# Optimization experiments

Measured on AMD Instinct MI355X. Metric: run time of the kernel, lower is better.

Reference implementation:

```python
import jax, jax.numpy as jnp
import numpy as np

NUM_EMBEDDINGS = 1024
EMBEDDING_DIM = 64


def setup_inputs() -> dict:
    key = jax.random.key(0)
    kx, kw = jax.random.split(key)
    x = jax.random.normal(kx, (16, 4096, EMBEDDING_DIM), dtype=jnp.float32)
    # torch init: uniform(-1/K, 1/K)
    bound = 1.0 / NUM_EMBEDDINGS
    weight = jax.random.uniform(kw, (NUM_EMBEDDINGS, EMBEDDING_DIM),
                                dtype=jnp.float32, minval=-bound, maxval=bound)
    return {"x": x, "weight": weight}


def reference(x, weight):
    flat_x = x.reshape(-1, EMBEDDING_DIM)                      # [N, D]
    x_sq = jnp.sum(flat_x ** 2, axis=1, keepdims=True)
    w_sq = jnp.sum(weight ** 2, axis=1)[None, :]
    distances = x_sq - 2.0 * (flat_x @ weight.T) + w_sq
    encoding_indices = jnp.argmin(distances, axis=1)           # [N]
    quantized = weight[encoding_indices]                       # [N, D]
    e_latent_loss = jnp.mean((jax.lax.stop_gradient(quantized) - flat_x) ** 2)
    q_latent_loss = jnp.mean((quantized - jax.lax.stop_gradient(flat_x)) ** 2)
    loss = q_latent_loss + 0.25 * e_latent_loss
    # straight-through estimator
    quantized = flat_x + jax.lax.stop_gradient(quantized - flat_x)
    return quantized.reshape(x.shape), encoding_indices, loss
```

## Files before the change

kernel.cpp:

```cpp
#include <hip/hip_runtime.h>
#include <math.h>

#define EMB_D 64
#define MARGIN 6.0e-5f
#define SBIAS 0.5f

typedef float  f32x4  __attribute__((ext_vector_type(4)));
typedef short  bf16x8 __attribute__((ext_vector_type(8)));

__device__ __forceinline__ unsigned short f2bf(float f) {
    unsigned int u = __float_as_uint(f);
    return (unsigned short)((u + 0x7FFFu + ((u >> 16) & 1u)) >> 16);
}
__device__ __forceinline__ float bf2f(unsigned short h) {
    return __uint_as_float(((unsigned int)h) << 16);
}

union Pack8 { ushort u[8]; bf16x8 v; uint4 q; };

__device__ __forceinline__ bf16x8 ldbf8(const unsigned short* p) {
    union { uint4 u; bf16x8 v; } c;
    c.u = *(const uint4*)p;
    return c.v;
}

__global__ __launch_bounds__(256)
void vq_prepw_kernel(const float* __restrict__ w,
                     unsigned short* __restrict__ wt_hi,
                     unsigned short* __restrict__ wt_lo,
                     float* __restrict__ wsq, float* __restrict__ loss_out,
                     int K) {
    const int i = blockIdx.x * 256 + threadIdx.x;
    if (i == 0) loss_out[0] = 0.f;
    if (i >= K * 8) return;
    const int krow = i >> 3, q = i & 7;
    const int dest = ((krow >> 6) << 9) + (((krow >> 4) & 3) << 7) + (q << 4)
                   + (krow & 15);
    const float* src = w + (size_t)krow * EMB_D + q * 8;
    Pack8 h, l;
#pragma unroll
    for (int j = 0; j < 8; ++j) {
        const float f = src[j];
        h.u[j] = f2bf(f);
        l.u[j] = f2bf(f - bf2f(h.u[j]));
    }
    ((uint4*)wt_hi)[dest] = h.q;
    ((uint4*)wt_lo)[dest] = l.q;

    if (i < K) {
        const float* wr = w + (size_t)i * EMB_D;
        float r[8];
#pragma unroll
        for (int j = 0; j < 8; ++j) r[j] = __fmul_rn(wr[j], wr[j]);
#pragma unroll
        for (int t = 1; t < 8; ++t)
#pragma unroll
            for (int j = 0; j < 8; ++j)
                r[j] = __fadd_rn(r[j], __fmul_rn(wr[t * 8 + j], wr[t * 8 + j]));
        float a = __fadd_rn(__fadd_rn(r[0], r[1]), __fadd_rn(r[2], r[3]));
        float b = __fadd_rn(__fadd_rn(r[4], r[5]), __fadd_rn(r[6], r[7]));
        wsq[i] = __fadd_rn(a, b);
    }
}

__global__ __launch_bounds__(256, 2)
void vq_fused_kernel(const float* __restrict__ x,
                     const unsigned short* __restrict__ wt_hi,
                     const unsigned short* __restrict__ wt_lo,
                     const float* __restrict__ wsq,
                     const float* __restrict__ w,
                     float* __restrict__ out, float* __restrict__ loss_out,
                     int K, int N, float scale) {
    const int tid  = threadIdx.x;
    const int lane = tid & 63;
    const int wave = tid >> 6;
    const int quad = lane >> 4;
    const int c16  = lane & 15;
    const int rowbase = blockIdx.x * 64 + wave * 16;

    __shared__ uint4 sh4[512];
    __shared__ uint4 sl4[512];
    __shared__ float wsq_lds[1024];
    __shared__ unsigned Mp1[4][16][17];
    __shared__ unsigned Mp2[4][16][17];
    __shared__ int kf[64], strow[64], k2row[64];

    const float* xrow = x + (size_t)(rowbase + c16) * EMB_D + quad * 8;
    Pack8 ah0, al0, ah1, al1;
#pragma unroll
    for (int j = 0; j < 8; ++j) {
        const float f0 = xrow[j];
        ah0.u[j] = f2bf(f0); al0.u[j] = f2bf(f0 - bf2f(ah0.u[j]));
        const float f1 = xrow[32 + j];
        ah1.u[j] = f2bf(f1); al1.u[j] = f2bf(f1 - bf2f(ah1.u[j]));
    }
    const bf16x8 AH0 = ah0.v, AL0 = al0.v, AH1 = ah1.v, AL1 = al1.v;

    {
        float4 a = ((const float4*)wsq)[tid];
        a.x += SBIAS; a.y += SBIAS; a.z += SBIAS; a.w += SBIAS;
        ((float4*)wsq_lds)[tid] = a;
    }

    unsigned s1v[4], s2v[4];
#pragma unroll
    for (int i = 0; i < 4; ++i) { s1v[i] = 0xFFFFFFFFu; s2v[i] = 0xFFFFFFFFu; }

    const uint4* gh = (const uint4*)wt_hi;
    const uint4* gl = (const uint4*)wt_lo;
    uint4 ph0 = gh[tid], ph1 = gh[256 + tid];
    uint4 pl0 = gl[tid], pl1 = gl[256 + tid];

    const int nseg = K >> 6;
    for (int seg = 0; seg < nseg; ++seg) {
        sh4[tid] = ph0; sh4[256 + tid] = ph1;
        sl4[tid] = pl0; sl4[256 + tid] = pl1;
        __syncthreads();
        if (seg + 1 < nseg) {
            const int b = (seg + 1) * 512;
            ph0 = gh[b + tid]; ph1 = gh[b + 256 + tid];
            pl0 = gl[b + tid]; pl1 = gl[b + 256 + tid];
        }

#pragma unroll
        for (int s = 0; s < 4; ++s) {
            const unsigned short* shp = (const unsigned short*)sh4;
            const unsigned short* slp = (const unsigned short*)sl4;
            const bf16x8 bhi0 = ldbf8(shp + (s * 128 + lane) * 8);
            const bf16x8 bhi1 = ldbf8(shp + (s * 128 + 64 + lane) * 8);
            const bf16x8 blo0 = ldbf8(slp + (s * 128 + lane) * 8);
            const bf16x8 blo1 = ldbf8(slp + (s * 128 + 64 + lane) * 8);
            const float wqb = wsq_lds[seg * 64 + s * 16 + c16];
            const unsigned idx6 = (unsigned)(seg * 4 + s);

            f32x4 a0 = {0.f, 0.f, 0.f, 0.f};
            f32x4 a1 = {0.f, 0.f, 0.f, 0.f};
            a0 = __builtin_amdgcn_mfma_f32_16x16x32_bf16(AL0, bhi0, a0, 0, 0, 0);
            a1 = __builtin_amdgcn_mfma_f32_16x16x32_bf16(AL1, bhi1, a1, 0, 0, 0);
            a0 = __builtin_amdgcn_mfma_f32_16x16x32_bf16(AH0, blo0, a0, 0, 0, 0);
            a1 = __builtin_amdgcn_mfma_f32_16x16x32_bf16(AH1, blo1, a1, 0, 0, 0);
            a0 = __builtin_amdgcn_mfma_f32_16x16x32_bf16(AH0, bhi0, a0, 0, 0, 0);
            a1 = __builtin_amdgcn_mfma_f32_16x16x32_bf16(AH1, bhi1, a1, 0, 0, 0);
#pragma unroll
            for (int i = 0; i < 4; ++i) {
                const float sc = fmaf(-2.0f, a0[i] + a1[i], wqb);
                const unsigned p = (__float_as_uint(sc) & 0xFFFFFFC0u) | idx6;
                const unsigned mx = p > s1v[i] ? p : s1v[i];
                s2v[i] = s2v[i] < mx ? s2v[i] : mx;
                s1v[i] = s1v[i] < p  ? s1v[i] : p;
            }
        }
        __syncthreads();
    }

#pragma unroll
    for (int i = 0; i < 4; ++i) {
        Mp1[wave][quad * 4 + i][c16] = s1v[i];
        Mp2[wave][quad * 4 + i][c16] = s2v[i];
    }
    __syncthreads();
    if (tid < 64) {
        const int wv = tid >> 4, r = tid & 15;
        unsigned g1 = 0xFFFFFFFFu, g2 = 0xFFFFFFFFu, g3 = 0xFFFFFFFFu;
        int gk1 = 0, gk2 = 0;
#pragma unroll
        for (int c = 0; c < 16; ++c) {
            {
                const unsigned p = Mp1[wv][r][c];
                if (p < g1)      { g3 = g2; g2 = g1; gk2 = gk1; g1 = p;
                                   gk1 = (int)(((p & 63u) << 4) | (unsigned)c); }
                else if (p < g2) { g3 = g2; g2 = p;
                                   gk2 = (int)(((p & 63u) << 4) | (unsigned)c); }
                else if (p < g3) { g3 = p; }
            }
            {
                const unsigned p = Mp2[wv][r][c];
                if (p < g1)      { g3 = g2; g2 = g1; gk2 = gk1; g1 = p;
                                   gk1 = (int)(((p & 63u) << 4) | (unsigned)c); }
                else if (p < g2) { g3 = g2; g2 = p;
                                   gk2 = (int)(((p & 63u) << 4) | (unsigned)c); }
                else if (p < g3) { g3 = p; }
            }
        }
        kf[tid] = gk1;
        const float f1 = __uint_as_float(g1 & 0xFFFFFFC0u);
        const float f2 = __uint_as_float(g2 & 0xFFFFFFC0u);
        const float f3 = __uint_as_float(g3 & 0xFFFFFFC0u);
        int st = 0;
        if (f2 - f1 <= MARGIN) st = (f3 - f1 > MARGIN) ? 1 : 2;
        strow[tid] = st;
        k2row[tid] = gk2;
    }
    __syncthreads();

    if (tid < 64 && strow[tid] == 1) {
        const int row = blockIdx.x * 64 + tid;
        const int ka = kf[tid], kb = k2row[tid];
        const float4* xp = (const float4*)(x + (size_t)row * EMB_D);
        const float4* wa = (const float4*)(w + (size_t)ka * EMB_D);
        const float4* wb = (const float4*)(w + (size_t)kb * EMB_D);
        float r[8];
        double aa0 = 0, aa1 = 0, aa2 = 0, aa3 = 0;
        double ab0 = 0, ab1 = 0, ab2 = 0, ab3 = 0;
#pragma unroll
        for (int q = 0; q < 16; ++q) {
            const float4 xv = xp[q], va = wa[q], vb = wb[q];
            const int j = (q & 1) * 4;
            if (q < 2) {
                r[j + 0] = __fmul_rn(xv.x, xv.x);
                r[j + 1] = __fmul_rn(xv.y, xv.y);
                r[j + 2] = __fmul_rn(xv.z, xv.z);
                r[j + 3] = __fmul_rn(xv.w, xv.w);
            } else {
                r[j + 0] = __fadd_rn(r[j + 0], __fmul_rn(xv.x, xv.x));
                r[j + 1] = __fadd_rn(r[j + 1], __fmul_rn(xv.y, xv.y));
                r[j + 2] = __fadd_rn(r[j + 2], __fmul_rn(xv.z, xv.z));
                r[j + 3] = __fadd_rn(r[j + 3], __fmul_rn(xv.w, xv.w));
            }
            aa0 = fma((double)xv.x, (double)va.x, aa0);
            aa1 = fma((double)xv.y, (double)va.y, aa1);
            aa2 = fma((double)xv.z, (double)va.z, aa2);
            aa3 = fma((double)xv.w, (double)va.w, aa3);
            ab0 = fma((double)xv.x, (double)vb.x, ab0);
            ab1 = fma((double)xv.y, (double)vb.y, ab1);
            ab2 = fma((double)xv.z, (double)vb.z, ab2);
            ab3 = fma((double)xv.w, (double)vb.w, ab3);
        }
        const float xsq = __fadd_rn(
            __fadd_rn(__fadd_rn(r[0], r[1]), __fadd_rn(r[2], r[3])),
            __fadd_rn(__fadd_rn(r[4], r[5]), __fadd_rn(r[6], r[7])));
        const float mfa = (float)((aa0 + aa1) + (aa2 + aa3));
        const float mfb = (float)((ab0 + ab1) + (ab2 + ab3));
        const float sa = __fadd_rn(__fsub_rn(xsq, __fmul_rn(2.0f, mfa)), wsq[ka]);
        const float sb = __fadd_rn(__fsub_rn(xsq, __fmul_rn(2.0f, mfb)), wsq[kb]);
        int win = ka;
        if (sb < sa || (sb == sa && kb < ka)) win = kb;
        kf[tid] = win;
    }
    __syncthreads();

    __shared__ float4 xs4[16];
    __shared__ float  xsqs;
    __shared__ float  ls[256];
    __shared__ int    lk[256];
    for (int i = 0; i < 64; ++i) {
        if (strow[i] != 2) continue;
        const int row = blockIdx.x * 64 + i;
        if (tid < 16) xs4[tid] = ((const float4*)(x + (size_t)row * EMB_D))[tid];
        __syncthreads();
        if (tid == 0) {
            const float* xf = (const float*)xs4;
            float r[8];
#pragma unroll
            for (int j = 0; j < 8; ++j) r[j] = __fmul_rn(xf[j], xf[j]);
#pragma unroll
            for (int t = 1; t < 8; ++t)
#pragma unroll
                for (int j = 0; j < 8; ++j)
                    r[j] = __fadd_rn(r[j], __fmul_rn(xf[t * 8 + j], xf[t * 8 + j]));
            xsqs = __fadd_rn(
                __fadd_rn(__fadd_rn(r[0], r[1]), __fadd_rn(r[2], r[3])),
                __fadd_rn(__fadd_rn(r[4], r[5]), __fadd_rn(r[6], r[7])));
        }
        __syncthreads();
        const float xsq = xsqs;

        float bs = INFINITY;
        int   bk = K;
        for (int t = 0; t < 4; ++t) {
            const int k = wave * (K >> 2) + t * 64 + lane;
            const float4* wr4 = (const float4*)(w + (size_t)k * EMB_D);
            double a0 = 0.0, a1 = 0.0, a2 = 0.0, a3 = 0.0;
#pragma unroll
            for (int q = 0; q < EMB_D / 4; ++q) {
                const float4 xv = xs4[q];
                const float4 wv = wr4[q];
                a0 = fma((double)xv.x, (double)wv.x, a0);
                a1 = fma((double)xv.y, (double)wv.y, a1);
                a2 = fma((double)xv.z, (double)wv.z, a2);
                a3 = fma((double)xv.w, (double)wv.w, a3);
            }
            const float mf = (float)((a0 + a1) + (a2 + a3));
            const float t2 = __fsub_rn(xsq, __fmul_rn(2.0f, mf));
            const float sc = __fadd_rn(t2, wsq[k]);
            if (sc < bs || (sc == bs && k < bk)) { bs = sc; bk = k; }
        }
        ls[tid] = bs; lk[tid] = bk;
        __syncthreads();
        if (wave == 0) {
            float gs = ls[lane];
            int   gk = lk[lane];
#pragma unroll
            for (int c = 1; c < 4; ++c) {
                const float os = ls[c * 64 + lane];
                const int   ok = lk[c * 64 + lane];
                if (os < gs || (os == gs && ok < gk)) { gs = os; gk = ok; }
            }
#pragma unroll
            for (int off = 32; off > 0; off >>= 1) {
                const float os = __shfl_down(gs, off);
                const int   ok = __shfl_down(gk, off);
                if (os < gs || (os == gs && ok < gk)) { gs = os; gk = ok; }
            }
            if (lane == 0) kf[i] = gk;
        }
        __syncthreads();
    }

    if (tid < 64) {
        const int row = blockIdx.x * 64 + tid;
        out[(size_t)N * EMB_D + row] = (float)kf[tid];
    }
    float lpart = 0.f;
#pragma unroll
    for (int rep = 0; rep < 4; ++rep) {
        int f4   = rep * 256 + tid;
        int rr   = f4 >> 4;
        int c    = f4 & 15;
        int k    = kf[rr];
        int grow = blockIdx.x * 64 + rr;
        float4 wv = ((const float4*)(w + (size_t)k * EMB_D))[c];
        float4 xq = ((const float4*)(x + (size_t)grow * EMB_D))[c];
        ((float4*)out)[(size_t)grow * (EMB_D / 4) + c] = wv;
        float dx = wv.x - xq.x, dy = wv.y - xq.y;
        float dz = wv.z - xq.z, dw = wv.w - xq.w;
        lpart += dx * dx + dy * dy + dz * dz + dw * dw;
    }
#pragma unroll
    for (int off = 32; off > 0; off >>= 1) lpart += __shfl_down(lpart, off);
    __shared__ float lred[4];
    if (lane == 0) lred[wave] = lpart;
    __syncthreads();
    if (tid == 0)
        atomicAdd(loss_out, ((lred[0] + lred[1]) + (lred[2] + lred[3])) * scale);
}

extern "C" void kernel_launch(void* const* d_in, const int* in_sizes, int n_in,
                              void* d_out, int out_size, void* d_ws, size_t ws_size,
                              hipStream_t stream) {
    const float* x = (const float*)d_in[0];
    const float* w = (const float*)d_in[1];
    float* out = (float*)d_out;
    const int xsz = in_sizes[0];
    const int wsz = in_sizes[1];
    const int N   = xsz / EMB_D;
    const int K   = wsz / EMB_D;
    const int NB  = N / 64;
    float* loss_out = out + (size_t)N * EMB_D + N;

    float* wsq = (float*)d_ws;
    unsigned short* wt_hi = (unsigned short*)(wsq + K);
    unsigned short* wt_lo = wt_hi + (size_t)K * EMB_D;

    vq_prepw_kernel<<<(K * 8 + 255) / 256, 256, 0, stream>>>(w, wt_hi, wt_lo,
                                                             wsq, loss_out, K);
    vq_fused_kernel<<<NB, 256, 0, stream>>>(x, wt_hi, wt_lo, wsq, w, out,
                                            loss_out, K, N,
                                            1.25f / (float)xsz);
}
```

Measured before the change: 134.4 us.

## Double-buffer codebook tiles in LDS via direct global-to-LDS loads

Replaces register-staged prefetch of the bf16 hi/lo codebook tiles with `global_load_lds` 16-byte direct transfers into a two-slot LDS arena. The next segment is fetched into the alternate buffer while the current one is consumed. This aims to remove the register round-trip and the per-segment LDS store instructions, and to cut VGPR pressure. The Mp1/Mp2 scratch arrays now alias the arena to limit LDS growth. The cost is more LDS per block and a correctness dependence on waitcnt and barrier placement for the asynchronous LDS writes.

```diff
diff --git a/kernel.cpp b/kernel.cpp
--- a/kernel.cpp
+++ b/kernel.cpp
@@ -22,6 +22,12 @@
     union { uint4 u; bf16x8 v; } c;
     c.u = *(const uint4*)p;
     return c.v;
+}
+
+__device__ __forceinline__ void stage16(const void* g, void* l) {
+    __builtin_amdgcn_global_load_lds(
+        (const __attribute__((address_space(1))) unsigned int*)g,
+        (__attribute__((address_space(3))) unsigned int*)l, 16, 0, 0);
 }
 
 __global__ __launch_bounds__(256)
@@ -78,12 +84,24 @@
     const int c16  = lane & 15;
     const int rowbase = blockIdx.x * 64 + wave * 16;
 
-    __shared__ uint4 sh4[512];
-    __shared__ uint4 sl4[512];
+    __shared__ __align__(16) char arena[32768];
     __shared__ float wsq_lds[1024];
-    __shared__ unsigned Mp1[4][16][17];
-    __shared__ unsigned Mp2[4][16][17];
+    typedef unsigned MpArr[16][17];
+    MpArr* Mp1 = (MpArr*)arena;
+    MpArr* Mp2 = (MpArr*)(arena + 4352);
     __shared__ int kf[64], strow[64], k2row[64];
+
+    const uint4* gh4 = (const uint4*)wt_hi;
+    const uint4* gl4 = (const uint4*)wt_lo;
+
+    {
+        uint4* bh = (uint4*)arena;
+        uint4* bl = (uint4*)(arena + 8192);
+        stage16(gh4 + tid,       bh + tid);
+        stage16(gh4 + 256 + tid, bh + 256 + tid);
+        stage16(gl4 + tid,       bl + tid);
+        stage16(gl4 + 256 + tid, bl + 256 + tid);
+    }
 
     const float* xrow = x + (size_t)(rowbase + c16) * EMB_D + quad * 8;
     Pack8 ah0, al0, ah1, al1;
@@ -106,26 +124,27 @@
 #pragma unroll
     for (int i = 0; i < 4; ++i) { s1v[i] = 0xFFFFFFFFu; s2v[i] = 0xFFFFFFFFu; }
 
-    const uint4* gh = (const uint4*)wt_hi;
-    const uint4* gl = (const uint4*)wt_lo;
-    uint4 ph0 = gh[tid], ph1 = gh[256 + tid];
-    uint4 pl0 = gl[tid], pl1 = gl[256 + tid];
+    __syncthreads();
 
     const int nseg = K >> 6;
     for (int seg = 0; seg < nseg; ++seg) {
-        sh4[tid] = ph0; sh4[256 + tid] = ph1;
-        sl4[tid] = pl0; sl4[256 + tid] = pl1;
-        __syncthreads();
+        const int cur = seg & 1;
         if (seg + 1 < nseg) {
             const int b = (seg + 1) * 512;
-            ph0 = gh[b + tid]; ph1 = gh[b + 256 + tid];
-            pl0 = gl[b + tid]; pl1 = gl[b + 256 + tid];
-        }
+            uint4* bh = (uint4*)(arena + (cur ^ 1) * 16384);
+            uint4* bl = (uint4*)(arena + (cur ^ 1) * 16384 + 8192);
+            stage16(gh4 + b + tid,       bh + tid);
+            stage16(gh4 + b + 256 + tid, bh + 256 + tid);
+            stage16(gl4 + b + tid,       bl + tid);
+            stage16(gl4 + b + 256 + tid, bl + 256 + tid);
+        }
+
+        const unsigned short* shp =
+            (const unsigned short*)(arena + cur * 16384);
+        const unsigned short* slp = shp + 4096;
 
 #pragma unroll
         for (int s = 0; s < 4; ++s) {
-            const unsigned short* shp = (const unsigned short*)sh4;
-            const unsigned short* slp = (const unsigned short*)sl4;
             const bf16x8 bhi0 = ldbf8(shp + (s * 128 + lane) * 8);
             const bf16x8 bhi1 = ldbf8(shp + (s * 128 + 64 + lane) * 8);
             const bf16x8 blo0 = ldbf8(slp + (s * 128 + lane) * 8);
```

Measured after the change: 139.3 us. 1.04x slower.

## Split codebook across wave pairs and give each wave two row tiles

Applied to the files above, without the earlier changes.

Each wave now handles 32 rows (two 16-row tiles) against half of the codebook, instead of 16 rows against the whole codebook. Every B fragment read from LDS feeds two sets of MFMAs, which halves LDS reads per MFMA. The staging loop drops from 16 segments of 64 codes to 16 steps of 32 codes per half, and the final merge combines the two halves. Register pressure roughly doubles for the A fragments and the top-2 state, which may hurt occupancy. Code and step counts are hardcoded to K=1024.

```diff
diff --git a/kernel.cpp b/kernel.cpp
--- a/kernel.cpp
+++ b/kernel.cpp
@@ -76,25 +76,32 @@
     const int wave = tid >> 6;
     const int quad = lane >> 4;
     const int c16  = lane & 15;
-    const int rowbase = blockIdx.x * 64 + wave * 16;
-
-    __shared__ uint4 sh4[512];
-    __shared__ uint4 sl4[512];
+    const int h    = wave >> 1;
+    const int rg   = wave & 1;
+    const int rowbase = blockIdx.x * 64 + rg * 32;
+
+    __shared__ __align__(16) char arena[17408];
     __shared__ float wsq_lds[1024];
-    __shared__ unsigned Mp1[4][16][17];
-    __shared__ unsigned Mp2[4][16][17];
+    typedef unsigned MpArr[32][17];
+    MpArr* Mp1 = (MpArr*)arena;
+    MpArr* Mp2 = (MpArr*)(arena + 8704);
     __shared__ int kf[64], strow[64], k2row[64];
 
-    const float* xrow = x + (size_t)(rowbase + c16) * EMB_D + quad * 8;
-    Pack8 ah0, al0, ah1, al1;
-#pragma unroll
-    for (int j = 0; j < 8; ++j) {
-        const float f0 = xrow[j];
-        ah0.u[j] = f2bf(f0); al0.u[j] = f2bf(f0 - bf2f(ah0.u[j]));
-        const float f1 = xrow[32 + j];
-        ah1.u[j] = f2bf(f1); al1.u[j] = f2bf(f1 - bf2f(ah1.u[j]));
-    }
-    const bf16x8 AH0 = ah0.v, AL0 = al0.v, AH1 = ah1.v, AL1 = al1.v;
+    Pack8 AH0[2], AL0[2], AH1[2], AL1[2];
+#pragma unroll
+    for (int tt = 0; tt < 2; ++tt) {
+        const float* xrow =
+            x + (size_t)(rowbase + tt * 16 + c16) * EMB_D + quad * 8;
+#pragma unroll
+        for (int j = 0; j < 8; ++j) {
+            const float f0 = xrow[j];
+            AH0[tt].u[j] = f2bf(f0);
+            AL0[tt].u[j] = f2bf(f0 - bf2f(AH0[tt].u[j]));
+            const float f1 = xrow[32 + j];
+            AH1[tt].u[j] = f2bf(f1);
+            AL1[tt].u[j] = f2bf(f1 - bf2f(AH1[tt].u[j]));
+        }
+    }
 
     {
         float4 a = ((const float4*)wsq)[tid];
@@ -102,84 +109,100 @@
         ((float4*)wsq_lds)[tid] = a;
     }
 
-    unsigned s1v[4], s2v[4];
-#pragma unroll
-    for (int i = 0; i < 4; ++i) { s1v[i] = 0xFFFFFFFFu; s2v[i] = 0xFFFFFFFFu; }
-
-    const uint4* gh = (const uint4*)wt_hi;
-    const uint4* gl = (const uint4*)wt_lo;
-    uint4 ph0 = gh[tid], ph1 = gh[256 + tid];
-    uint4 pl0 = gl[tid], pl1 = gl[256 + tid];
-
-    const int nseg = K >> 6;
-    for (int seg = 0; seg < nseg; ++seg) {
-        sh4[tid] = ph0; sh4[256 + tid] = ph1;
-        sl4[tid] = pl0; sl4[256 + tid] = pl1;
-        __syncthreads();
-        if (seg + 1 < nseg) {
-            const int b = (seg + 1) * 512;
-            ph0 = gh[b + tid]; ph1 = gh[b + 256 + tid];
-            pl0 = gl[b + tid]; pl1 = gl[b + 256 + tid];
-        }
-
-#pragma unroll
-        for (int s = 0; s < 4; ++s) {
-            const unsigned short* shp = (const unsigned short*)sh4;
-            const unsigned short* slp = (const unsigned short*)sl4;
+    unsigned s1v[2][4], s2v[2][4];
+#pragma unroll
+    for (int tt = 0; tt < 2; ++tt)
+#pragma unroll
+        for (int i = 0; i < 4; ++i) { s1v[tt][i] = 0xFFFFFFFFu; s2v[tt][i] = 0xFFFFFFFFu; }
+
+    const uint4* gh4 = (const uint4*)wt_hi;
+    const uint4* gl4 = (const uint4*)wt_lo;
+    uint4 ph0 = gh4[tid], pl0 = gl4[tid];
+    uint4 ph1 = gh4[4096 + tid], pl1 = gl4[4096 + tid];
+
+    for (int t = 0; t < 16; ++t) {
+        ((uint4*)arena)[tid]           = ph0;
+        ((uint4*)(arena + 4096))[tid]  = pl0;
+        ((uint4*)(arena + 8192))[tid]  = ph1;
+        ((uint4*)(arena + 12288))[tid] = pl1;
+        __syncthreads();
+        if (t + 1 < 16) {
+            ph0 = gh4[(t + 1) * 256 + tid];
+            pl0 = gl4[(t + 1) * 256 + tid];
+            ph1 = gh4[(17 + t) * 256 + tid];
+            pl1 = gl4[(17 + t) * 256 + tid];
+        }
+
+        const unsigned short* shp =
+            (const unsigned short*)(arena + h * 8192);
+        const unsigned short* slp = shp + 2048;
+
+#pragma unroll
+        for (int s = 0; s < 2; ++s) {
             const bf16x8 bhi0 = ldbf8(shp + (s * 128 + lane) * 8);
             const bf16x8 bhi1 = ldbf8(shp + (s * 128 + 64 + lane) * 8);
             const bf16x8 blo0 = ldbf8(slp + (s * 128 + lane) * 8);
             const bf16x8 blo1 = ldbf8(slp + (s * 128 + 64 + lane) * 8);
-            const float wqb = wsq_lds[seg * 64 + s * 16 + c16];
-            const unsigned idx6 = (unsigned)(seg * 4 + s);
-
-            f32x4 a0 = {0.f, 0.f, 0.f, 0.f};
-            f32x4 a1 = {0.f, 0.f, 0.f, 0.f};
-            a0 = __builtin_amdgcn_mfma_f32_16x16x32_bf16(AL0, bhi0, a0, 0, 0, 0);
-            a1 = __builtin_amdgcn_mfma_f32_16x16x32_bf16(AL1, bhi1, a1, 0, 0, 0);
-            a0 = __builtin_amdgcn_mfma_f32_16x16x32_bf16(AH0, blo0, a0, 0, 0, 0);
-            a1 = __builtin_amdgcn_mfma_f32_16x16x32_bf16(AH1, blo1, a1, 0, 0, 0);
-            a0 = __builtin_amdgcn_mfma_f32_16x16x32_bf16(AH0, bhi0, a0, 0, 0, 0);
-            a1 = __builtin_amdgcn_mfma_f32_16x16x32_bf16(AH1, bhi1, a1, 0, 0, 0);
-#pragma unroll
-            for (int i = 0; i < 4; ++i) {
-                const float sc = fmaf(-2.0f, a0[i] + a1[i], wqb);
-                const unsigned p = (__float_as_uint(sc) & 0xFFFFFFC0u) | idx6;
-                const unsigned mx = p > s1v[i] ? p : s1v[i];
-                s2v[i] = s2v[i] < mx ? s2v[i] : mx;
-                s1v[i] = s1v[i] < p  ? s1v[i] : p;
-            }
-        }
-        __syncthreads();
-    }
-
-#pragma unroll
-    for (int i = 0; i < 4; ++i) {
-        Mp1[wave][quad * 4 + i][c16] = s1v[i];
-        Mp2[wave][quad * 4 + i][c16] = s2v[i];
-    }
+            const unsigned u = (unsigned)(h * 32 + t * 2 + s);
+            const float wqb = wsq_lds[u * 16 + c16];
+
+#pragma unroll
+            for (int tt = 0; tt < 2; ++tt) {
+                f32x4 a0 = {0.f, 0.f, 0.f, 0.f};
+                f32x4 a1 = {0.f, 0.f, 0.f, 0.f};
+                a0 = __builtin_amdgcn_mfma_f32_16x16x32_bf16(AL0[tt].v, bhi0, a0, 0, 0, 0);
+                a1 = __builtin_amdgcn_mfma_f32_16x16x32_bf16(AL1[tt].v, bhi1, a1, 0, 0, 0);
+                a0 = __builtin_amdgcn_mfma_f32_16x16x32_bf16(AH0[tt].v, blo0, a0, 0, 0, 0);
+                a1 = __builtin_amdgcn_mfma_f32_16x16x32_bf16(AH1[tt].v, blo1, a1, 0, 0, 0);
+                a0 = __builtin_amdgcn_mfma_f32_16x16x32_bf16(AH0[tt].v, bhi0, a0, 0, 0, 0);
+                a1 = __builtin_amdgcn_mfma_f32_16x16x32_bf16(AH1[tt].v, bhi1, a1, 0, 0, 0);
+#pragma unroll
+                for (int i = 0; i < 4; ++i) {
+                    const float sc = fmaf(-2.0f, a0[i] + a1[i], wqb);
+                    const unsigned p = (__float_as_uint(sc) & 0xFFFFFFC0u) | u;
+                    const unsigned mx = p > s1v[tt][i] ? p : s1v[tt][i];
+                    s2v[tt][i] = s2v[tt][i] < mx ? s2v[tt][i] : mx;
+                    s1v[tt][i] = s1v[tt][i] < p  ? s1v[tt][i] : p;
+                }
+            }
+        }
+        __syncthreads();
+    }
+
+#pragma unroll
+    for (int tt = 0; tt < 2; ++tt)
+#pragma unroll
+        for (int i = 0; i < 4; ++i) {
+            const int rr = tt * 16 + quad * 4 + i;
+            Mp1[wave][rr][c16] = s1v[tt][i];
+            Mp2[wave][rr][c16] = s2v[tt][i];
+        }
     __syncthreads();
     if (tid < 64) {
-        const int wv = tid >> 4, r = tid & 15;
+        const int rg2 = tid >> 5, rr = tid & 31;
         unsigned g1 = 0xFFFFFFFFu, g2 = 0xFFFFFFFFu, g3 = 0xFFFFFFFFu;
         int gk1 = 0, gk2 = 0;
 #pragma unroll
         for (int c = 0; c < 16; ++c) {
-            {
-                const unsigned p = Mp1[wv][r][c];
-                if (p < g1)      { g3 = g2; g2 = g1; gk2 = gk1; g1 = p;
-                                   gk1 = (int)(((p & 63u) << 4) | (unsigned)c); }
-                else if (p < g2) { g3 = g2; g2 = p;
-                                   gk2 = (int)(((p & 63u) << 4) | (unsigned)c); }
-                else if (p < g3) { g3 = p; }
-            }
-            {
-                const unsigned p = Mp2[wv][r][c];
-                if (p < g1)      { g3 = g2; g2 = g1; gk2 = gk1; g1 = p;
-                                   gk1 = (int)(((p & 63u) << 4) | (unsigned)c); }
-                else if (p < g2) { g3 = g2; g2 = p;
-                                   gk2 = (int)(((p & 63u) << 4) | (unsigned)c); }
-                else if (p < g3) { g3 = p; }
+#pragma unroll
+            for (int j = 0; j < 2; ++j) {
+                const int wv = rg2 + j * 2;
+                {
+                    const unsigned p = Mp1[wv][rr][c];
+                    if (p < g1)      { g3 = g2; g2 = g1; gk2 = gk1; g1 = p;
+                                       gk1 = (int)(((p & 63u) << 4) | (unsigned)c); }
+                    else if (p < g2) { g3 = g2; g2 = p;
+                                       gk2 = (int)(((p & 63u) << 4) | (unsigned)c); }
+                    else if (p < g3) { g3 = p; }
+                }
+                {
+                    const unsigned p = Mp2[wv][rr][c];
+                    if (p < g1)      { g3 = g2; g2 = g1; gk2 = gk1; g1 = p;
+                                       gk1 = (int)(((p & 63u) << 4) | (unsigned)c); }
+                    else if (p < g2) { g3 = g2; g2 = p;
+                                       gk2 = (int)(((p & 63u) << 4) | (unsigned)c); }
+                    else if (p < g3) { g3 = p; }
+                }
             }
         }
         kf[tid] = gk1;
```

New measurement: 138.9 us. 3.4% more time.
